# Kernel optimization log

Hardware: AMD Instinct MI355X
Metric: run time of the kernel (lower is better)

Reference implementation:

```python
import jax, jax.numpy as jnp
import numpy as np

H = 128  # hidden size
IN = 12  # input size
OUT = 4  # output classes


def _lstm_scan(gates_x, Whh, B, dtype, collect_ys):
    """gates_x: [T,B,4H] precomputed input-to-hidden gates (with biases).
    PyTorch gate order: i, f, g, o."""
    h0 = jnp.zeros((B, H), dtype)
    c0 = jnp.zeros((B, H), dtype)

    def step(carry, gx):
        h, c = carry
        g = gx + h @ Whh.T  # [B,4H]
        i, f, gg, o = jnp.split(g, 4, axis=-1)
        c = jax.nn.sigmoid(f) * c + jax.nn.sigmoid(i) * jnp.tanh(gg)
        h = jax.nn.sigmoid(o) * jnp.tanh(c)
        return (h, c), (h if collect_ys else None)

    (hT, cT), hs = jax.lax.scan(step, (h0, c0), gates_x)
    return hs, hT


def setup_inputs() -> dict:
    key = jax.random.key(0)
    ks = jax.random.split(key, 12)
    B, T = 256, 2048
    s = 1.0 / np.sqrt(H)  # torch LSTM/Linear init scale
    u = lambda k, shape: jax.random.uniform(k, shape, jnp.float32, -s, s)
    return {
        "x": jax.random.normal(ks[0], (B, T, IN), jnp.float32),
        "W_ih_l0": u(ks[1], (4 * H, IN)),
        "W_hh_l0": u(ks[2], (4 * H, H)),
        "b_ih_l0": u(ks[3], (4 * H,)),
        "b_hh_l0": u(ks[4], (4 * H,)),
        "W_ih_l1": u(ks[5], (4 * H, H)),
        "W_hh_l1": u(ks[6], (4 * H, H)),
        "b_ih_l1": u(ks[7], (4 * H,)),
        "b_hh_l1": u(ks[8], (4 * H,)),
        "W_out": u(ks[9], (OUT, H)),
        "b_out": u(ks[10], (OUT,)),
    }


def reference(x, W_ih_l0, W_hh_l0, b_ih_l0, b_hh_l0,
              W_ih_l1, W_hh_l1, b_ih_l1, b_hh_l1, W_out, b_out):
    B = x.shape[0]
    # layer 0: precompute all input projections at once -> [T,B,4H]
    gx0 = jnp.einsum('bti,gi->tbg', x, W_ih_l0) + b_ih_l0 + b_hh_l0
    hs0, _ = _lstm_scan(gx0, W_hh_l0, B, x.dtype, collect_ys=True)  # [T,B,H]
    # layer 1: only final hidden state is needed (r_out[:, -1] == h_T)
    gx1 = jnp.einsum('tbh,gh->tbg', hs0, W_ih_l1) + b_ih_l1 + b_hh_l1
    _, hT = _lstm_scan(gx1, W_hh_l1, B, x.dtype, collect_ys=False)  # [B,H]
    return hT @ W_out.T + b_out  # [B,4]
```

## Files before the change

### kernel.cpp

```cpp
#include <hip/hip_runtime.h>
#include <cstdint>
#include <cstddef>

#define H      128
#define IN_    12
#define GATES  512
#define B_     256
#define T_     2048
#define TCMAX  512
#define TT     64
#define PS     520

#define REP32(M) M(0) M(1) M(2) M(3) M(4) M(5) M(6) M(7) M(8) M(9) M(10) M(11) \
  M(12) M(13) M(14) M(15) M(16) M(17) M(18) M(19) M(20) M(21) M(22) M(23) \
  M(24) M(25) M(26) M(27) M(28) M(29) M(30) M(31)

__device__ __forceinline__ float sigmoidf_(float x) {
    return 1.f / (1.f + __expf(-x));
}
__device__ __forceinline__ float tanhf_(float x) {
    return 2.f / (1.f + __expf(-2.f * x)) - 1.f;
}
__device__ __forceinline__ float dot4f(float4 w, float4 h, float a) {
    return fmaf(w.x, h.x, fmaf(w.y, h.y, fmaf(w.z, h.z, fmaf(w.w, h.w, a))));
}

template<bool IS_L0>
__device__ __forceinline__ void scan_body(
    int b, const float* __restrict__ x_or_gx, const float* __restrict__ Wih,
    const float* __restrict__ Whh, const float* __restrict__ bih,
    const float* __restrict__ bhh, float* __restrict__ hs0,
    float* __restrict__ state, int tc, int chunk, float* smem)
{
    const int tid = threadIdx.x;
    const int ks  = tid >> 7;
    const int q   = tid & 127;

    float* sh_part = smem;
    float* sh_h    = smem + 8 * PS;
    float* sh_x    = sh_h + H;

#define LOADW(i) \
    const float4* wr##i = (const float4*)(Whh + (size_t)(4*q+i)*H + 16*ks); \
    float4 w##i##0 = wr##i[0], w##i##1 = wr##i[1], w##i##2 = wr##i[2], w##i##3 = wr##i[3];
    LOADW(0) LOADW(1) LOADW(2) LOADW(3)
#undef LOADW

    float4 wx0 = {0,0,0,0}, wx1 = {0,0,0,0}, wx2 = {0,0,0,0}, wx3 = {0,0,0,0};
    if constexpr (IS_L0) {
        if (ks >= 1 && ks <= 3) {
            wx0 = *(const float4*)(Wih + (size_t)(4*q+0)*IN_ + 4*(ks-1));
            wx1 = *(const float4*)(Wih + (size_t)(4*q+1)*IN_ + 4*(ks-1));
            wx2 = *(const float4*)(Wih + (size_t)(4*q+2)*IN_ + 4*(ks-1));
            wx3 = *(const float4*)(Wih + (size_t)(4*q+3)*IN_ + 4*(ks-1));
        }
        const float* xs = x_or_gx + ((size_t)b * T_ + (size_t)chunk * tc) * IN_;
        for (int i = tid; i < tc * IN_; i += 1024) sh_x[i] = xs[i];
    }

    float bias0 = 0, bias1 = 0, bias2 = 0, bias3 = 0;
    float cur0 = 0, cur1 = 0, cur2 = 0, cur3 = 0;
    float hreg = 0.f, creg = 0.f;
    const float* gxb = nullptr;
    if constexpr (!IS_L0) gxb = x_or_gx + (size_t)b * tc * GATES;

    if (tid < H) {
        if constexpr (IS_L0) {
            bias0 = bih[tid]       + bhh[tid];
            bias1 = bih[tid + 128] + bhh[tid + 128];
            bias2 = bih[tid + 256] + bhh[tid + 256];
            bias3 = bih[tid + 384] + bhh[tid + 384];
        } else {
            cur0 = gxb[tid]; cur1 = gxb[tid + 128];
            cur2 = gxb[tid + 256]; cur3 = gxb[tid + 384];
        }
        if (chunk) { hreg = state[b*2*H + tid]; creg = state[b*2*H + H + tid]; }
        sh_h[tid] = hreg;
    }
    __syncthreads();

    float* hs_out = nullptr;
    if constexpr (IS_L0) hs_out = hs0 + (size_t)b * tc * H;

    const float4* sh4 = (const float4*)sh_h;
    const int i0 = tid & 3, q0 = tid >> 2;

    for (int t = 0; t < tc; ++t) {
        float n0 = 0, n1 = 0, n2 = 0, n3 = 0;
        if constexpr (!IS_L0) {
            if (tid < H) {
                int tn = (t + 1 < tc) ? t + 1 : t;
                const float* gp = gxb + (size_t)tn * GATES;
                n0 = gp[tid]; n1 = gp[tid + 128];
                n2 = gp[tid + 256]; n3 = gp[tid + 384];
            }
        }
        float4 hA = sh4[4*ks], hB = sh4[4*ks+1], hC = sh4[4*ks+2], hD = sh4[4*ks+3];
        float a0 = dot4f(w03,hD, dot4f(w02,hC, dot4f(w01,hB, dot4f(w00,hA, 0.f))));
        float a1 = dot4f(w13,hD, dot4f(w12,hC, dot4f(w11,hB, dot4f(w10,hA, 0.f))));
        float a2 = dot4f(w23,hD, dot4f(w22,hC, dot4f(w21,hB, dot4f(w20,hA, 0.f))));
        float a3 = dot4f(w33,hD, dot4f(w32,hC, dot4f(w31,hB, dot4f(w30,hA, 0.f))));
        if constexpr (IS_L0) {
            if (ks >= 1 && ks <= 3) {
                float4 xq = *(const float4*)(sh_x + t * IN_ + 4*(ks-1));
                a0 = dot4f(wx0, xq, a0); a1 = dot4f(wx1, xq, a1);
                a2 = dot4f(wx2, xq, a2); a3 = dot4f(wx3, xq, a3);
            }
        }
        sh_part[ks*PS + 0*128 + q] = a0;
        sh_part[ks*PS + 1*128 + q] = a1;
        sh_part[ks*PS + 2*128 + q] = a2;
        sh_part[ks*PS + 3*128 + q] = a3;
        __syncthreads();

        if (tid < H) {
            float p0, p1, p2, p3;
            {
                const float* pb = sh_part + i0*128 + q0;
#define RSUM(m, dst) { \
                float s = pb[32*m]; \
                s += pb[32*m + 1*PS]; s += pb[32*m + 2*PS]; s += pb[32*m + 3*PS]; \
                s += pb[32*m + 4*PS]; s += pb[32*m + 5*PS]; s += pb[32*m + 6*PS]; \
                s += pb[32*m + 7*PS]; dst = s; }
                RSUM(0, p0) RSUM(1, p1) RSUM(2, p2) RSUM(3, p3)
#undef RSUM
            }
            float gi, gf, gg, go;
            if constexpr (IS_L0) {
                gi = p0 + bias0; gf = p1 + bias1; gg = p2 + bias2; go = p3 + bias3;
            } else {
                gi = p0 + cur0; gf = p1 + cur1; gg = p2 + cur2; go = p3 + cur3;
                cur0 = n0; cur1 = n1; cur2 = n2; cur3 = n3;
            }
            creg = fmaf(sigmoidf_(gf), creg, sigmoidf_(gi) * tanhf_(gg));
            hreg = sigmoidf_(go) * tanhf_(creg);
            sh_h[tid] = hreg;
            if constexpr (IS_L0) hs_out[(size_t)t * H + tid] = hreg;
        }
        __syncthreads();
    }
    if (tid < H) { state[b*2*H + tid] = hreg; state[b*2*H + H + tid] = creg; }
}

__global__ __launch_bounds__(1024) void lstm_scan_l0(
    const float* __restrict__ x, const float* __restrict__ Wih,
    const float* __restrict__ Whh, const float* __restrict__ bih,
    const float* __restrict__ bhh, float* __restrict__ hs0,
    float* __restrict__ state, int tc, int chunk)
{
    extern __shared__ float smem[];
    scan_body<true>(blockIdx.x, x, Wih, Whh, bih, bhh, hs0, state, tc, chunk, smem);
}

__global__ __launch_bounds__(1024) void lstm_scan_l1(
    const float* __restrict__ gx, const float* __restrict__ Whh,
    float* __restrict__ state, int tc, int chunk)
{
    extern __shared__ float smem[];
    scan_body<false>(blockIdx.x, gx, nullptr, Whh, nullptr, nullptr,
                     nullptr, state, tc, chunk, smem);
}

__global__ __launch_bounds__(1024) void lstm_pair(
    const float* __restrict__ x, const float* __restrict__ Wih0,
    const float* __restrict__ Whh0, const float* __restrict__ bih0,
    const float* __restrict__ bhh0, float* __restrict__ hs0,
    float* __restrict__ st0, int c0,
    const float* __restrict__ gx1, const float* __restrict__ Whh1,
    float* __restrict__ st1, int c1, int tc)
{
    extern __shared__ float smem[];
    if (blockIdx.x < B_) {
        scan_body<true>(blockIdx.x, x, Wih0, Whh0, bih0, bhh0, hs0, st0,
                        tc, c0, smem);
    } else {
        scan_body<false>(blockIdx.x - B_, gx1, nullptr, Whh1, nullptr, nullptr,
                         nullptr, st1, tc, c1, smem);
    }
}

typedef __attribute__((ext_vector_type(16))) float f16x;

__global__ __launch_bounds__(512)
void gx1_gemm(const float* __restrict__ hs0, const float* __restrict__ Wih,
              const float* __restrict__ bih, const float* __restrict__ bhh,
              float* __restrict__ gx, int tc)
{
    const int b  = blockIdx.x;
    const int t0 = blockIdx.y * TT;
    const int g  = threadIdx.x;

#define LWG(j) float4 w##j = ((const float4*)(Wih + (size_t)g * H))[j];
    REP32(LWG)
#undef LWG
    const float biasg = bih[g] + bhh[g];

    const float* hp = hs0 + ((size_t)b * tc + t0) * H;
    float* gxo = gx + ((size_t)b * tc + t0) * GATES + g;

    for (int t = 0; t < TT; ++t) {
        const float* hpt = hp + (size_t)t * H;
        float a0 = biasg, a1 = 0.f, a2 = 0.f, a3 = 0.f;

        f16x h0, h1, h2, h3;
        asm volatile(
            "s_load_dwordx16 %0, %4, 0x0\n\t"
            "s_load_dwordx16 %1, %4, 0x40\n\t"
            "s_load_dwordx16 %2, %4, 0x80\n\t"
            "s_load_dwordx16 %3, %4, 0xc0\n\t"
            "s_waitcnt lgkmcnt(0)"
            : "=s"(h0), "=s"(h1), "=s"(h2), "=s"(h3)
            : "s"(hpt));
#define Q4(hv, j0, j1, j2, j3) { \
        a0 = fmaf(w##j0.x, hv.s0, a0); a1 = fmaf(w##j0.y, hv.s1, a1); \
        a2 = fmaf(w##j0.z, hv.s2, a2); a3 = fmaf(w##j0.w, hv.s3, a3); \
        a0 = fmaf(w##j1.x, hv.s4, a0); a1 = fmaf(w##j1.y, hv.s5, a1); \
        a2 = fmaf(w##j1.z, hv.s6, a2); a3 = fmaf(w##j1.w, hv.s7, a3); \
        a0 = fmaf(w##j2.x, hv.s8, a0); a1 = fmaf(w##j2.y, hv.s9, a1); \
        a2 = fmaf(w##j2.z, hv.sa, a2); a3 = fmaf(w##j2.w, hv.sb, a3); \
        a0 = fmaf(w##j3.x, hv.sc, a0); a1 = fmaf(w##j3.y, hv.sd, a1); \
        a2 = fmaf(w##j3.z, hv.se, a2); a3 = fmaf(w##j3.w, hv.sf, a3); }
        Q4(h0, 0, 1, 2, 3)    Q4(h1, 4, 5, 6, 7)
        Q4(h2, 8, 9, 10, 11)  Q4(h3, 12, 13, 14, 15)

        asm volatile(
            "s_load_dwordx16 %0, %4, 0x100\n\t"
            "s_load_dwordx16 %1, %4, 0x140\n\t"
            "s_load_dwordx16 %2, %4, 0x180\n\t"
            "s_load_dwordx16 %3, %4, 0x1c0\n\t"
            "s_waitcnt lgkmcnt(0)"
            : "=s"(h0), "=s"(h1), "=s"(h2), "=s"(h3)
            : "s"(hpt));
        Q4(h0, 16, 17, 18, 19)  Q4(h1, 20, 21, 22, 23)
        Q4(h2, 24, 25, 26, 27)  Q4(h3, 28, 29, 30, 31)
#undef Q4

        gxo[(size_t)t * GATES] = (a0 + a1) + (a2 + a3);
    }
}

__global__ void out_proj(const float* __restrict__ state1,
                         const float* __restrict__ Wout,
                         const float* __restrict__ bout,
                         float* __restrict__ out)
{
    const int b = blockIdx.x, j = threadIdx.x;
    __shared__ float sh[H];
    if (j < H) sh[j] = state1[b*2*H + j];
    __syncthreads();
    if (j < 4) {
        float a = bout[j];
        for (int k = 0; k < H; ++k) a = fmaf(Wout[j*H + k], sh[k], a);
        out[b*4 + j] = a;
    }
}

extern "C" void kernel_launch(void* const* d_in, const int* in_sizes, int n_in,
                              void* d_out, int out_size, void* d_ws, size_t ws_size,
                              hipStream_t stream)
{
    const float* x    = (const float*)d_in[0];
    const float* Wih0 = (const float*)d_in[1];
    const float* Whh0 = (const float*)d_in[2];
    const float* bih0 = (const float*)d_in[3];
    const float* bhh0 = (const float*)d_in[4];
    const float* Wih1 = (const float*)d_in[5];
    const float* Whh1 = (const float*)d_in[6];
    const float* bih1 = (const float*)d_in[7];
    const float* bhh1 = (const float*)d_in[8];
    const float* Wout = (const float*)d_in[9];
    const float* bout = (const float*)d_in[10];

    int tc = TT;
    for (int cand = TCMAX; cand >= TT; cand >>= 1) {
        size_t need = (size_t)2 * B_ * 2 * H * 4
                    + (size_t)B_ * cand * H * 4
                    + (size_t)B_ * cand * GATES * 4;
        if (need <= ws_size) { tc = cand; break; }
    }

    float* ws  = (float*)d_ws;
    float* st0 = ws;
    float* st1 = st0 + (size_t)B_ * 2 * H;
    float* hs0 = st1 + (size_t)B_ * 2 * H;
    float* gx1 = hs0 + (size_t)B_ * tc * H;

    const size_t shm_l0 = (size_t)(8 * PS + H + tc * IN_) * 4;
    const size_t shm_l1 = (size_t)(8 * PS + H) * 4;

    const int nchunks = T_ / tc;

    lstm_scan_l0<<<B_, 1024, shm_l0, stream>>>(
        x, Wih0, Whh0, bih0, bhh0, hs0, st0, tc, 0);
    gx1_gemm<<<dim3(B_, tc / TT), 512, 0, stream>>>(
        hs0, Wih1, bih1, bhh1, gx1, tc);
    for (int c = 1; c < nchunks; ++c) {
        lstm_pair<<<2 * B_, 1024, shm_l0, stream>>>(
            x, Wih0, Whh0, bih0, bhh0, hs0, st0, c,
            gx1, Whh1, st1, c - 1, tc);
        gx1_gemm<<<dim3(B_, tc / TT), 512, 0, stream>>>(
            hs0, Wih1, bih1, bhh1, gx1, tc);
    }
    lstm_scan_l1<<<B_, 1024, shm_l1, stream>>>(gx1, Whh1, st1, tc, nchunks - 1);
    out_proj<<<B_, 128, 0, stream>>>(st1, Wout, bout, (float*)d_out);
}
```

Before: 5.655 ms.

## Broadcast hidden state via readlane, remap gate rows, drop layer-pair pipelining

Each thread now reads the hidden state with one float2 LDS load per lane and broadcasts the elements it needs via readlane, instead of four float4 LDS loads per thread. Whh rows are remapped so each thread owns gate q of all four gate types, which lets the partial sums be written and reduced as float4 without the padded stride. The fused lstm_pair kernel that ran layer 0 and layer 1 concurrently is removed; chunks now run l0, gemm and l1 in sequence, and the scan kernels are pinned to 4 waves per EU. This cuts LDS traffic and bank conflicts in the recurrent step but gives up the overlap between the two layers and adds more launches.

```diff
diff --git a/kernel.cpp b/kernel.cpp
--- a/kernel.cpp
+++ b/kernel.cpp
@@ -9,11 +9,12 @@
 #define T_     2048
 #define TCMAX  512
 #define TT     64
-#define PS     520
 
 #define REP32(M) M(0) M(1) M(2) M(3) M(4) M(5) M(6) M(7) M(8) M(9) M(10) M(11) \
   M(12) M(13) M(14) M(15) M(16) M(17) M(18) M(19) M(20) M(21) M(22) M(23) \
   M(24) M(25) M(26) M(27) M(28) M(29) M(30) M(31)
+
+#define RLF(v, l) __int_as_float(__builtin_amdgcn_readlane(__float_as_int(v), (l)))
 
 __device__ __forceinline__ float sigmoidf_(float x) {
     return 1.f / (1.f + __expf(-x));
@@ -32,27 +33,29 @@
     const float* __restrict__ bhh, float* __restrict__ hs0,
     float* __restrict__ state, int tc, int chunk, float* smem)
 {
-    const int tid = threadIdx.x;
-    const int ks  = tid >> 7;
-    const int q   = tid & 127;
+    const int tid  = threadIdx.x;
+    const int lane = tid & 63;
+    const int q    = tid & 127;
+    const int ksu  = __builtin_amdgcn_readfirstlane(threadIdx.x >> 7);
+    const int lb   = 8 * ksu;
 
     float* sh_part = smem;
-    float* sh_h    = smem + 8 * PS;
+    float* sh_h    = smem + 8 * 512;
     float* sh_x    = sh_h + H;
 
 #define LOADW(i) \
-    const float4* wr##i = (const float4*)(Whh + (size_t)(4*q+i)*H + 16*ks); \
-    float4 w##i##0 = wr##i[0], w##i##1 = wr##i[1], w##i##2 = wr##i[2], w##i##3 = wr##i[3];
+    const float4* wr##i = (const float4*)(Whh + (size_t)(i * H + q) * H + 16 * ksu); \
+    float4 w##i##a = wr##i[0], w##i##b = wr##i[1], w##i##c = wr##i[2], w##i##d = wr##i[3];
     LOADW(0) LOADW(1) LOADW(2) LOADW(3)
 #undef LOADW
 
     float4 wx0 = {0,0,0,0}, wx1 = {0,0,0,0}, wx2 = {0,0,0,0}, wx3 = {0,0,0,0};
     if constexpr (IS_L0) {
-        if (ks >= 1 && ks <= 3) {
-            wx0 = *(const float4*)(Wih + (size_t)(4*q+0)*IN_ + 4*(ks-1));
-            wx1 = *(const float4*)(Wih + (size_t)(4*q+1)*IN_ + 4*(ks-1));
-            wx2 = *(const float4*)(Wih + (size_t)(4*q+2)*IN_ + 4*(ks-1));
-            wx3 = *(const float4*)(Wih + (size_t)(4*q+3)*IN_ + 4*(ks-1));
+        if (ksu >= 1 && ksu <= 3) {
+            wx0 = *(const float4*)(Wih + (size_t)(0 * H + q) * IN_ + 4 * (ksu - 1));
+            wx1 = *(const float4*)(Wih + (size_t)(1 * H + q) * IN_ + 4 * (ksu - 1));
+            wx2 = *(const float4*)(Wih + (size_t)(2 * H + q) * IN_ + 4 * (ksu - 1));
+            wx3 = *(const float4*)(Wih + (size_t)(3 * H + q) * IN_ + 4 * (ksu - 1));
         }
         const float* xs = x_or_gx + ((size_t)b * T_ + (size_t)chunk * tc) * IN_;
         for (int i = tid; i < tc * IN_; i += 1024) sh_x[i] = xs[i];
@@ -82,8 +85,8 @@
     float* hs_out = nullptr;
     if constexpr (IS_L0) hs_out = hs0 + (size_t)b * tc * H;
 
-    const float4* sh4 = (const float4*)sh_h;
-    const int i0 = tid & 3, q0 = tid >> 2;
+    float4* sp4w = (float4*)sh_part;
+    const float4* sp4 = (const float4*)sh_part;
 
     for (int t = 0; t < tc; ++t) {
         float n0 = 0, n1 = 0, n2 = 0, n3 = 0;
@@ -95,41 +98,45 @@
                 n2 = gp[tid + 256]; n3 = gp[tid + 384];
             }
         }
-        float4 hA = sh4[4*ks], hB = sh4[4*ks+1], hC = sh4[4*ks+2], hD = sh4[4*ks+3];
-        float a0 = dot4f(w03,hD, dot4f(w02,hC, dot4f(w01,hB, dot4f(w00,hA, 0.f))));
-        float a1 = dot4f(w13,hD, dot4f(w12,hC, dot4f(w11,hB, dot4f(w10,hA, 0.f))));
-        float a2 = dot4f(w23,hD, dot4f(w22,hC, dot4f(w21,hB, dot4f(w20,hA, 0.f))));
-        float a3 = dot4f(w33,hD, dot4f(w32,hC, dot4f(w31,hB, dot4f(w30,hA, 0.f))));
+        float2 hl = ((const float2*)sh_h)[lane];
+        float he0 = RLF(hl.x, lb+0), ho0 = RLF(hl.y, lb+0);
+        float he1 = RLF(hl.x, lb+1), ho1 = RLF(hl.y, lb+1);
+        float he2 = RLF(hl.x, lb+2), ho2 = RLF(hl.y, lb+2);
+        float he3 = RLF(hl.x, lb+3), ho3 = RLF(hl.y, lb+3);
+        float he4 = RLF(hl.x, lb+4), ho4 = RLF(hl.y, lb+4);
+        float he5 = RLF(hl.x, lb+5), ho5 = RLF(hl.y, lb+5);
+        float he6 = RLF(hl.x, lb+6), ho6 = RLF(hl.y, lb+6);
+        float he7 = RLF(hl.x, lb+7), ho7 = RLF(hl.y, lb+7);
+
+        float a0 = 0.f, a1 = 0.f, a2 = 0.f, a3 = 0.f;
+#define ROWFMA(i) \
+  a##i = fmaf(w##i##a.x, he0, fmaf(w##i##a.y, ho0, fmaf(w##i##a.z, he1, fmaf(w##i##a.w, ho1, a##i)))); \
+  a##i = fmaf(w##i##b.x, he2, fmaf(w##i##b.y, ho2, fmaf(w##i##b.z, he3, fmaf(w##i##b.w, ho3, a##i)))); \
+  a##i = fmaf(w##i##c.x, he4, fmaf(w##i##c.y, ho4, fmaf(w##i##c.z, he5, fmaf(w##i##c.w, ho5, a##i)))); \
+  a##i = fmaf(w##i##d.x, he6, fmaf(w##i##d.y, ho6, fmaf(w##i##d.z, he7, fmaf(w##i##d.w, ho7, a##i))));
+        ROWFMA(0) ROWFMA(1) ROWFMA(2) ROWFMA(3)
+#undef ROWFMA
         if constexpr (IS_L0) {
-            if (ks >= 1 && ks <= 3) {
-                float4 xq = *(const float4*)(sh_x + t * IN_ + 4*(ks-1));
+            if (ksu >= 1 && ksu <= 3) {
+                float4 xq = *(const float4*)(sh_x + t * IN_ + 4 * (ksu - 1));
                 a0 = dot4f(wx0, xq, a0); a1 = dot4f(wx1, xq, a1);
                 a2 = dot4f(wx2, xq, a2); a3 = dot4f(wx3, xq, a3);
             }
         }
-        sh_part[ks*PS + 0*128 + q] = a0;
-        sh_part[ks*PS + 1*128 + q] = a1;
-        sh_part[ks*PS + 2*128 + q] = a2;
-        sh_part[ks*PS + 3*128 + q] = a3;
+        float4 av; av.x = a0; av.y = a1; av.z = a2; av.w = a3;
+        sp4w[(ksu << 7) + q] = av;
         __syncthreads();
 
         if (tid < H) {
-            float p0, p1, p2, p3;
-            {
-                const float* pb = sh_part + i0*128 + q0;
-#define RSUM(m, dst) { \
-                float s = pb[32*m]; \
-                s += pb[32*m + 1*PS]; s += pb[32*m + 2*PS]; s += pb[32*m + 3*PS]; \
-                s += pb[32*m + 4*PS]; s += pb[32*m + 5*PS]; s += pb[32*m + 6*PS]; \
-                s += pb[32*m + 7*PS]; dst = s; }
-                RSUM(0, p0) RSUM(1, p1) RSUM(2, p2) RSUM(3, p3)
-#undef RSUM
-            }
+            float4 s = sp4[tid];
+#define RQ(m) { float4 v = sp4[m * 128 + tid]; s.x += v.x; s.y += v.y; s.z += v.z; s.w += v.w; }
+            RQ(1) RQ(2) RQ(3) RQ(4) RQ(5) RQ(6) RQ(7)
+#undef RQ
             float gi, gf, gg, go;
             if constexpr (IS_L0) {
-                gi = p0 + bias0; gf = p1 + bias1; gg = p2 + bias2; go = p3 + bias3;
+                gi = s.x + bias0; gf = s.y + bias1; gg = s.z + bias2; go = s.w + bias3;
             } else {
-                gi = p0 + cur0; gf = p1 + cur1; gg = p2 + cur2; go = p3 + cur3;
+                gi = s.x + cur0; gf = s.y + cur1; gg = s.z + cur2; go = s.w + cur3;
                 cur0 = n0; cur1 = n1; cur2 = n2; cur3 = n3;
             }
             creg = fmaf(sigmoidf_(gf), creg, sigmoidf_(gi) * tanhf_(gg));
@@ -142,7 +149,9 @@
     if (tid < H) { state[b*2*H + tid] = hreg; state[b*2*H + H + tid] = creg; }
 }
 
-__global__ __launch_bounds__(1024) void lstm_scan_l0(
+__global__ __launch_bounds__(1024)
+__attribute__((amdgpu_waves_per_eu(4, 4)))
+void lstm_scan_l0(
     const float* __restrict__ x, const float* __restrict__ Wih,
     const float* __restrict__ Whh, const float* __restrict__ bih,
     const float* __restrict__ bhh, float* __restrict__ hs0,
@@ -152,31 +161,15 @@
     scan_body<true>(blockIdx.x, x, Wih, Whh, bih, bhh, hs0, state, tc, chunk, smem);
 }
 
-__global__ __launch_bounds__(1024) void lstm_scan_l1(
+__global__ __launch_bounds__(1024)
+__attribute__((amdgpu_waves_per_eu(4, 4)))
+void lstm_scan_l1(
     const float* __restrict__ gx, const float* __restrict__ Whh,
     float* __restrict__ state, int tc, int chunk)
 {
     extern __shared__ float smem[];
     scan_body<false>(blockIdx.x, gx, nullptr, Whh, nullptr, nullptr,
                      nullptr, state, tc, chunk, smem);
-}
-
-__global__ __launch_bounds__(1024) void lstm_pair(
-    const float* __restrict__ x, const float* __restrict__ Wih0,
-    const float* __restrict__ Whh0, const float* __restrict__ bih0,
-    const float* __restrict__ bhh0, float* __restrict__ hs0,
-    float* __restrict__ st0, int c0,
-    const float* __restrict__ gx1, const float* __restrict__ Whh1,
-    float* __restrict__ st1, int c1, int tc)
-{
-    extern __shared__ float smem[];
-    if (blockIdx.x < B_) {
-        scan_body<true>(blockIdx.x, x, Wih0, Whh0, bih0, bhh0, hs0, st0,
-                        tc, c0, smem);
-    } else {
-        scan_body<false>(blockIdx.x - B_, gx1, nullptr, Whh1, nullptr, nullptr,
-                         nullptr, st1, tc, c1, smem);
-    }
 }
 
 typedef __attribute__((ext_vector_type(16))) float f16x;
@@ -285,22 +278,16 @@
     float* hs0 = st1 + (size_t)B_ * 2 * H;
     float* gx1 = hs0 + (size_t)B_ * tc * H;
 
-    const size_t shm_l0 = (size_t)(8 * PS + H + tc * IN_) * 4;
-    const size_t shm_l1 = (size_t)(8 * PS + H) * 4;
+    const size_t shm_l0 = (size_t)(8 * 512 + H + tc * IN_) * 4;
+    const size_t shm_l1 = (size_t)(8 * 512 + H) * 4;
 
     const int nchunks = T_ / tc;
-
-    lstm_scan_l0<<<B_, 1024, shm_l0, stream>>>(
-        x, Wih0, Whh0, bih0, bhh0, hs0, st0, tc, 0);
-    gx1_gemm<<<dim3(B_, tc / TT), 512, 0, stream>>>(
-        hs0, Wih1, bih1, bhh1, gx1, tc);
-    for (int c = 1; c < nchunks; ++c) {
-        lstm_pair<<<2 * B_, 1024, shm_l0, stream>>>(
-            x, Wih0, Whh0, bih0, bhh0, hs0, st0, c,
-            gx1, Whh1, st1, c - 1, tc);
+    for (int c = 0; c < nchunks; ++c) {
+        lstm_scan_l0<<<B_, 1024, shm_l0, stream>>>(
+            x, Wih0, Whh0, bih0, bhh0, hs0, st0, tc, c);
         gx1_gemm<<<dim3(B_, tc / TT), 512, 0, stream>>>(
             hs0, Wih1, bih1, bhh1, gx1, tc);
-    }
-    lstm_scan_l1<<<B_, 1024, shm_l1, stream>>>(gx1, Whh1, st1, tc, nchunks - 1);
+        lstm_scan_l1<<<B_, 1024, shm_l1, stream>>>(gx1, Whh1, st1, tc, c);
+    }
     out_proj<<<B_, 128, 0, stream>>>(st1, Wout, bout, (float*)d_out);
 }
```

New measurement: 5.753 ms. No clear change (+1.7%).
